# Kernel tuning notes

Measured on AMD Instinct MI355X. Metric: run time of the kernel, lower is better.

Reference implementation:

```python
import jax, jax.numpy as jnp
import numpy as np

HEADS = 4
DIM_HEAD = 32
EPS = 1e-5

def _layernorm(x, g, b):
    mu = jnp.mean(x, axis=-1, keepdims=True)
    var = jnp.var(x, axis=-1, keepdims=True)
    return (x - mu) * jax.lax.rsqrt(var + EPS) * g + b

def setup_inputs() -> dict:
    key = jax.random.key(0)
    ks = jax.random.split(key, 8)
    B, C, H, W = 16, 256, 32, 32
    N = H * W
    inner = HEADS * DIM_HEAD  # 128
    s = lambda d: 1.0 / np.sqrt(d)
    return {
        "x": jax.random.normal(ks[0], (B, C, H, W), jnp.float32),
        "pos_embedding": jax.random.normal(ks[1], (1, N, C), jnp.float32),
        "w_qkv": jax.random.normal(ks[2], (C, inner * 3), jnp.float32) * s(C),
        "w_out": jax.random.normal(ks[3], (inner, C), jnp.float32) * s(inner),
        "b_out": jnp.zeros((C,), jnp.float32),
        "w_ff1": jax.random.normal(ks[4], (C, inner), jnp.float32) * s(C),
        "b_ff1": jnp.zeros((inner,), jnp.float32),
        "w_ff2": jax.random.normal(ks[5], (inner, C), jnp.float32) * s(inner),
        "b_ff2": jnp.zeros((C,), jnp.float32),
        "g1": jnp.ones((C,), jnp.float32),
        "beta1": jnp.zeros((C,), jnp.float32),
        "g2": jnp.ones((C,), jnp.float32),
        "beta2": jnp.zeros((C,), jnp.float32),
    }

def reference(x, pos_embedding, w_qkv, w_out, b_out, w_ff1, b_ff1, w_ff2, b_ff2, g1, beta1, g2, beta2):
    b, c, h, w = x.shape
    n = h * w
    tok = jnp.transpose(x.reshape(b, c, n), (0, 2, 1))  # [b, n, c]
    tok = tok + pos_embedding  # (dropout is identity at eval)
    # attention
    qkv = _layernorm(tok, g1, beta1) @ w_qkv  # [b, n, 3*inner]
    qkv = qkv.reshape(b, n, 3, HEADS, DIM_HEAD)
    q, k, v = qkv[:, :, 0], qkv[:, :, 1], qkv[:, :, 2]  # [b, n, h, d]
    scale = DIM_HEAD ** -0.5
    dots = jnp.einsum('bihd,bjhd->bhij', q, k) * scale
    attn = jax.nn.softmax(dots, axis=-1)
    out = jnp.einsum('bhij,bjhd->bihd', attn, v).reshape(b, n, HEADS * DIM_HEAD)
    tok = out @ w_out + b_out + tok
    # ffn
    hdn = jax.nn.gelu(_layernorm(tok, g2, beta2) @ w_ff1 + b_ff1, approximate=False)
    tok = hdn @ w_ff2 + b_ff2 + tok
    return jnp.transpose(tok, (0, 2, 1)).reshape(b, c, h, w)
```

## Files before the change

### kernel.cpp

```cpp
#include <hip/hip_runtime.h>
#include <hip/hip_bf16.h>
#include <math.h>

#define B_     16
#define C_     256
#define N_     1024
#define HEADS_ 4
#define DH_    32
#define INNER_ 128
#define EPS_   1e-5f

typedef __attribute__((ext_vector_type(8))) short bf16x8;
typedef __attribute__((ext_vector_type(4))) float f32x4;

__device__ __forceinline__ ushort f2bf(float f) {
  union { float f; unsigned u; } v; v.f = f;
  unsigned u = v.u;
  return (ushort)((u + 0x7fffu + ((u >> 16) & 1u)) >> 16);
}
__device__ __forceinline__ float bf2f(ushort u) {
  union { unsigned u; float f; } v; v.u = ((unsigned)u) << 16;
  return v.f;
}
__device__ __forceinline__ unsigned cvt_pk_bf16(float lo, float hi) {
  unsigned r;
  asm("v_cvt_pk_bf16_f32 %0, %1, %2" : "=v"(r) : "v"(lo), "v"(hi));
  return r;
}

#define QSCALE_ 0.2550348652979437f

__global__ __launch_bounds__(256) void k_wconv(
    const float* __restrict__ wqkv, const float* __restrict__ wout,
    const float* __restrict__ wff1, const float* __restrict__ wff2,
    ushort* __restrict__ wqkvT, ushort* __restrict__ woutT,
    ushort* __restrict__ wff1T, ushort* __restrict__ wff2T) {
  int i = blockIdx.x * 256 + threadIdx.x;
  if (i < 98304) {
    int k = i / 384, n = i % 384;
    wqkvT[n * 256 + k] = f2bf(wqkv[i]);
    return;
  }
  i -= 98304;
  if (i < 32768) {
    int k = i / 256, n = i % 256;
    woutT[n * 128 + k] = f2bf(wout[i]);
    return;
  }
  i -= 32768;
  if (i < 32768) {
    int k = i / 128, n = i % 128;
    wff1T[n * 256 + k] = f2bf(wff1[i]);
    return;
  }
  i -= 32768;
  {
    int k = i / 256, n = i % 256;
    wff2T[n * 128 + k] = f2bf(wff2[i]);
  }
}

union KFusedSmem {
  float  xs[C_][68];
  ushort xnl[64][264];
};

__global__ __launch_bounds__(512) void k_fused(
    const float* __restrict__ x, const float* __restrict__ pos,
    const float* __restrict__ g1, const float* __restrict__ beta1,
    const ushort* __restrict__ wqkvT, ushort* __restrict__ tokb,
    ushort* __restrict__ qb, ushort* __restrict__ kb, ushort* __restrict__ vtb) {
  const int b  = blockIdx.x >> 4;
  const int n0 = (blockIdx.x & 15) << 6;
  const int t  = threadIdx.x;
  __shared__ KFusedSmem u;

  {
    const int nq = t & 15, cq = t >> 4;
#pragma unroll
    for (int i = 0; i < 8; ++i) {
      const int c = i * 32 + cq;
      const float4 v = *reinterpret_cast<const float4*>(
          &x[((size_t)b * C_ + c) * N_ + n0 + 4 * nq]);
      *reinterpret_cast<float4*>(&u.xs[c][4 * nq]) = v;
    }
  }
  __syncthreads();

  {
    const int tl = t >> 3, sub = t & 7, c0 = sub * 32;
    const int n = n0 + tl;
    float v[32];
#pragma unroll
    for (int i = 0; i < 32; ++i) v[i] = u.xs[c0 + i][tl];
#pragma unroll
    for (int j = 0; j < 8; ++j) {
      const float4 p = *reinterpret_cast<const float4*>(&pos[(size_t)n * C_ + c0 + 4 * j]);
      v[4*j] += p.x; v[4*j+1] += p.y; v[4*j+2] += p.z; v[4*j+3] += p.w;
    }
    float s = 0.f;
#pragma unroll
    for (int i = 0; i < 32; ++i) s += v[i];
    s += __shfl_xor(s, 1); s += __shfl_xor(s, 2); s += __shfl_xor(s, 4);
    const float mu = s * (1.f / C_);
    float sq = 0.f;
#pragma unroll
    for (int i = 0; i < 32; ++i) { const float d = v[i] - mu; sq += d * d; }
    sq += __shfl_xor(sq, 1); sq += __shfl_xor(sq, 2); sq += __shfl_xor(sq, 4);
    const float rs = rsqrtf(sq * (1.f / C_) + EPS_);

    ushort* tokrow = &tokb[((size_t)b * N_ + n) * C_ + c0];
    ushort xn_local[32];
#pragma unroll
    for (int j = 0; j < 8; ++j) {
      ushort4 tu;
      tu.x = f2bf(v[4*j]);   tu.y = f2bf(v[4*j+1]);
      tu.z = f2bf(v[4*j+2]); tu.w = f2bf(v[4*j+3]);
      *reinterpret_cast<ushort4*>(&tokrow[4 * j]) = tu;
      const float4 g  = *reinterpret_cast<const float4*>(&g1[c0 + 4 * j]);
      const float4 be = *reinterpret_cast<const float4*>(&beta1[c0 + 4 * j]);
      xn_local[4*j]   = f2bf((v[4*j]   - mu) * rs * g.x + be.x);
      xn_local[4*j+1] = f2bf((v[4*j+1] - mu) * rs * g.y + be.y);
      xn_local[4*j+2] = f2bf((v[4*j+2] - mu) * rs * g.z + be.z);
      xn_local[4*j+3] = f2bf((v[4*j+3] - mu) * rs * g.w + be.w);
    }
    __syncthreads();
#pragma unroll
    for (int j = 0; j < 8; ++j)
      *reinterpret_cast<ushort4*>(&u.xnl[tl][c0 + 4 * j]) =
          *reinterpret_cast<ushort4*>(&xn_local[4 * j]);
  }
  __syncthreads();

  {
    const int w = t >> 6, lane = t & 63;
    const int li = lane & 15, g = lane >> 4;
#pragma unroll
    for (int mf = 0; mf < 3; ++mf) {
      const int chb = w * 48 + mf * 16;
      bf16x8 Af[8];
#pragma unroll
      for (int ks = 0; ks < 8; ++ks)
        Af[ks] = *reinterpret_cast<const bf16x8*>(
            &wqkvT[(size_t)(chb + li) * C_ + ks * 32 + 8 * g]);
#pragma unroll
      for (int nf = 0; nf < 4; ++nf) {
        bf16x8 Bf[8];
#pragma unroll
        for (int ks = 0; ks < 8; ++ks)
          Bf[ks] = *reinterpret_cast<const bf16x8*>(&u.xnl[nf * 16 + li][ks * 32 + 8 * g]);
        f32x4 acc = {0.f, 0.f, 0.f, 0.f};
#pragma unroll
        for (int ks = 0; ks < 8; ++ks)
          acc = __builtin_amdgcn_mfma_f32_16x16x32_bf16(Af[ks], Bf[ks], acc, 0, 0, 0);
        const int nn = n0 + nf * 16 + li;
        const int ch0 = chb + 4 * g;
        if (ch0 < 128) {
          const int h = ch0 >> 5, dh = ch0 & 31;
          ushort4 uq;
          uq.x = f2bf(acc[0] * QSCALE_); uq.y = f2bf(acc[1] * QSCALE_);
          uq.z = f2bf(acc[2] * QSCALE_); uq.w = f2bf(acc[3] * QSCALE_);
          *reinterpret_cast<ushort4*>(&qb[(((size_t)(b * HEADS_ + h)) * N_ + nn) * DH_ + dh]) = uq;
        } else if (ch0 < 256) {
          const int c2 = ch0 - 128, h = c2 >> 5, dh = c2 & 31;
          ushort4 uk;
          uk.x = f2bf(acc[0]); uk.y = f2bf(acc[1]); uk.z = f2bf(acc[2]); uk.w = f2bf(acc[3]);
          *reinterpret_cast<ushort4*>(&kb[(((size_t)(b * HEADS_ + h)) * N_ + nn) * DH_ + dh]) = uk;
        } else {
          const int c2 = ch0 - 256, h = c2 >> 5, dh = c2 & 31;
          ushort* base = &vtb[(((size_t)(b * HEADS_ + h)) * DH_ + dh) * N_ + nn];
          base[0] = f2bf(acc[0]); base[N_] = f2bf(acc[1]);
          base[2 * N_] = f2bf(acc[2]); base[3 * N_] = f2bf(acc[3]);
        }
      }
    }
  }
}

__global__ __launch_bounds__(256) void k_attn_mlp(
    const ushort* __restrict__ qb, const ushort* __restrict__ kb,
    const ushort* __restrict__ vtb, const ushort* __restrict__ tokb,
    const ushort* __restrict__ woutT, const float* __restrict__ b_out,
    const ushort* __restrict__ wff1T, const float* __restrict__ b_ff1,
    const ushort* __restrict__ wff2T, const float* __restrict__ b_ff2,
    const float* __restrict__ g2, const float* __restrict__ beta2,
    float* __restrict__ out) {
  const int b   = blockIdx.x >> 5;
  const int tt  = blockIdx.x & 31;
  const int nq0 = tt * 32;
  const int tid = threadIdx.x;
  const int w = tid >> 6, lane = tid & 63;
  const int qi = lane & 15, g = lane >> 4;

  __shared__ __align__(16) union {
    ushort P[4][2][16][72];
    float  t2s[32][260];
  } u1;
  __shared__ __align__(16) ushort xn2[32][264];
  __shared__ __align__(16) union {
    ushort aos[32][136];
    ushort hsb[32][136];
  } u2;

  {
    const int bh = b * HEADS_ + w;
    const ushort* Kb = kb  + (size_t)bh * N_ * DH_;
    const ushort* Vt = vtb + (size_t)bh * DH_ * N_;

    bf16x8 qf[2];
#pragma unroll
    for (int G = 0; G < 2; ++G)
      qf[G] = *reinterpret_cast<const bf16x8*>(
          qb + ((size_t)bh * N_ + nq0 + G * 16 + qi) * DH_ + 8 * g);

    f32x4 acc[2][2];
#pragma unroll
    for (int G = 0; G < 2; ++G)
#pragma unroll
      for (int d = 0; d < 2; ++d)
#pragma unroll
        for (int r = 0; r < 4; ++r) acc[G][d][r] = 0.f;
    float l[2] = {0.f, 0.f};

    bf16x8 kf[4], vf[2][2];
#pragma unroll
    for (int kt = 0; kt < 4; ++kt)
      kf[kt] = *reinterpret_cast<const bf16x8*>(
          Kb + (size_t)(kt * 16 + qi) * DH_ + 8 * g);
#pragma unroll
    for (int c = 0; c < 2; ++c)
#pragma unroll
      for (int d = 0; d < 2; ++d)
        vf[c][d] = *reinterpret_cast<const bf16x8*>(
            Vt + (size_t)(d * 16 + qi) * N_ + c * 32 + 8 * g);

    for (int jt = 0; jt < 16; ++jt) {
      const int kn = (jt < 15 ? jt + 1 : 15) * 64;
      bf16x8 kfn[4], vfn[2][2];
#pragma unroll
      for (int kt = 0; kt < 4; ++kt)
        kfn[kt] = *reinterpret_cast<const bf16x8*>(
            Kb + (size_t)(kn + kt * 16 + qi) * DH_ + 8 * g);
#pragma unroll
      for (int c = 0; c < 2; ++c)
#pragma unroll
        for (int d = 0; d < 2; ++d)
          vfn[c][d] = *reinterpret_cast<const bf16x8*>(
              Vt + (size_t)(d * 16 + qi) * N_ + kn + c * 32 + 8 * g);

      f32x4 s[2][4];
#pragma unroll
      for (int G = 0; G < 2; ++G)
#pragma unroll
        for (int kt = 0; kt < 4; ++kt) {
          f32x4 z = {0.f, 0.f, 0.f, 0.f};
          s[G][kt] = __builtin_amdgcn_mfma_f32_16x16x32_bf16(kf[kt], qf[G], z, 0, 0, 0);
        }

#pragma unroll
      for (int G = 0; G < 2; ++G) {
        float psum = 0.f;
#pragma unroll
        for (int kt = 0; kt < 4; ++kt) {
          const float p0 = exp2f(s[G][kt][0]);
          const float p1 = exp2f(s[G][kt][1]);
          const float p2 = exp2f(s[G][kt][2]);
          const float p3 = exp2f(s[G][kt][3]);
          psum += (p0 + p1) + (p2 + p3);
          uint2 dw;
          dw.x = cvt_pk_bf16(p0, p1);
          dw.y = cvt_pk_bf16(p2, p3);
          *reinterpret_cast<uint2*>(&u1.P[w][G][qi][kt * 16 + 4 * g]) = dw;
        }
        l[G] += psum;
      }

#pragma unroll
      for (int c = 0; c < 2; ++c) {
        const bf16x8 pf0 = *reinterpret_cast<const bf16x8*>(&u1.P[w][0][qi][c * 32 + 8 * g]);
        const bf16x8 pf1 = *reinterpret_cast<const bf16x8*>(&u1.P[w][1][qi][c * 32 + 8 * g]);
#pragma unroll
        for (int d = 0; d < 2; ++d) {
          acc[0][d] = __builtin_amdgcn_mfma_f32_16x16x32_bf16(vf[c][d], pf0, acc[0][d], 0, 0, 0);
          acc[1][d] = __builtin_amdgcn_mfma_f32_16x16x32_bf16(vf[c][d], pf1, acc[1][d], 0, 0, 0);
        }
      }

#pragma unroll
      for (int kt = 0; kt < 4; ++kt) kf[kt] = kfn[kt];
#pragma unroll
      for (int c = 0; c < 2; ++c)
#pragma unroll
        for (int d = 0; d < 2; ++d) vf[c][d] = vfn[c][d];
    }

#pragma unroll
    for (int G = 0; G < 2; ++G) {
      float lg = l[G];
      lg += __shfl_xor(lg, 16);
      lg += __shfl_xor(lg, 32);
      const float inv = 1.f / lg;
      const int nloc = G * 16 + qi;
#pragma unroll
      for (int d = 0; d < 2; ++d) {
        ushort4 uo;
        uo.x = f2bf(acc[G][d][0] * inv);
        uo.y = f2bf(acc[G][d][1] * inv);
        uo.z = f2bf(acc[G][d][2] * inv);
        uo.w = f2bf(acc[G][d][3] * inv);
        *reinterpret_cast<ushort4*>(&u2.aos[nloc][w * 32 + d * 16 + 4 * g]) = uo;
      }
    }
  }
  __syncthreads();

  const int li = qi;

  {
    bf16x8 Af[2][4];
#pragma unroll
    for (int mf = 0; mf < 2; ++mf)
#pragma unroll
      for (int ks = 0; ks < 4; ++ks)
        Af[mf][ks] = *reinterpret_cast<const bf16x8*>(&u2.aos[mf * 16 + li][ks * 32 + 8 * g]);
#pragma unroll
    for (int nf = 0; nf < 4; ++nf) {
      const int n = w * 64 + nf * 16;
      bf16x8 Bf[4];
#pragma unroll
      for (int ks = 0; ks < 4; ++ks)
        Bf[ks] = *reinterpret_cast<const bf16x8*>(
            &woutT[(size_t)(n + li) * INNER_ + ks * 32 + 8 * g]);
#pragma unroll
      for (int mf = 0; mf < 2; ++mf) {
        f32x4 acc = {0.f, 0.f, 0.f, 0.f};
#pragma unroll
        for (int ks = 0; ks < 4; ++ks)
          acc = __builtin_amdgcn_mfma_f32_16x16x32_bf16(Af[mf][ks], Bf[ks], acc, 0, 0, 0);
        const int nch = n + li;
        const int tl0 = mf * 16 + 4 * g;
        const float bo = b_out[nch];
#pragma unroll
        for (int r = 0; r < 4; ++r)
          u1.t2s[tl0 + r][nch] =
              acc[r] + bo + bf2f(tokb[((size_t)b * N_ + nq0 + tl0 + r) * C_ + nch]);
      }
    }
  }
  __syncthreads();

  {
    const int tl = tid >> 3, c0 = (tid & 7) * 32;
    float v[32];
#pragma unroll
    for (int j = 0; j < 8; ++j) {
      const float4 t4 = *reinterpret_cast<const float4*>(&u1.t2s[tl][c0 + 4 * j]);
      v[4*j] = t4.x; v[4*j+1] = t4.y; v[4*j+2] = t4.z; v[4*j+3] = t4.w;
    }
    float s = 0.f;
#pragma unroll
    for (int i = 0; i < 32; ++i) s += v[i];
    s += __shfl_xor(s, 1); s += __shfl_xor(s, 2); s += __shfl_xor(s, 4);
    const float mu = s * (1.f / C_);
    float sq = 0.f;
#pragma unroll
    for (int i = 0; i < 32; ++i) { const float d = v[i] - mu; sq += d * d; }
    sq += __shfl_xor(sq, 1); sq += __shfl_xor(sq, 2); sq += __shfl_xor(sq, 4);
    const float rs = rsqrtf(sq * (1.f / C_) + EPS_);
#pragma unroll
    for (int j = 0; j < 8; ++j) {
      const float4 gg = *reinterpret_cast<const float4*>(&g2[c0 + 4 * j]);
      const float4 be = *reinterpret_cast<const float4*>(&beta2[c0 + 4 * j]);
      ushort4 uu;
      uu.x = f2bf((v[4*j]   - mu) * rs * gg.x + be.x);
      uu.y = f2bf((v[4*j+1] - mu) * rs * gg.y + be.y);
      uu.z = f2bf((v[4*j+2] - mu) * rs * gg.z + be.z);
      uu.w = f2bf((v[4*j+3] - mu) * rs * gg.w + be.w);
      *reinterpret_cast<ushort4*>(&xn2[tl][c0 + 4 * j]) = uu;
    }
  }
  __syncthreads();

  {
    bf16x8 Af[2][8];
#pragma unroll
    for (int mf = 0; mf < 2; ++mf)
#pragma unroll
      for (int ks = 0; ks < 8; ++ks)
        Af[mf][ks] = *reinterpret_cast<const bf16x8*>(&xn2[mf * 16 + li][ks * 32 + 8 * g]);
#pragma unroll
    for (int nf = 0; nf < 2; ++nf) {
      const int n = w * 32 + nf * 16;
      bf16x8 Bf[8];
#pragma unroll
      for (int ks = 0; ks < 8; ++ks)
        Bf[ks] = *reinterpret_cast<const bf16x8*>(
            &wff1T[(size_t)(n + li) * C_ + ks * 32 + 8 * g]);
#pragma unroll
      for (int mf = 0; mf < 2; ++mf) {
        f32x4 acc = {0.f, 0.f, 0.f, 0.f};
#pragma unroll
        for (int ks = 0; ks < 8; ++ks)
          acc = __builtin_amdgcn_mfma_f32_16x16x32_bf16(Af[mf][ks], Bf[ks], acc, 0, 0, 0);
        const int nch = n + li;
        const int tl0 = mf * 16 + 4 * g;
        const float bf1 = b_ff1[nch];
#pragma unroll
        for (int r = 0; r < 4; ++r) {
          float hv = acc[r] + bf1;
          hv = 0.5f * hv * (1.f + erff(hv * 0.70710678118654752f));
          u2.hsb[tl0 + r][nch] = f2bf(hv);
        }
      }
    }
  }
  __syncthreads();

  {
    bf16x8 Af[2][4];
#pragma unroll
    for (int mf = 0; mf < 2; ++mf)
#pragma unroll
      for (int ks = 0; ks < 4; ++ks)
        Af[mf][ks] = *reinterpret_cast<const bf16x8*>(&u2.hsb[mf * 16 + li][ks * 32 + 8 * g]);
#pragma unroll
    for (int nf = 0; nf < 4; ++nf) {
      const int n = w * 64 + nf * 16;
      bf16x8 Bf[4];
#pragma unroll
      for (int ks = 0; ks < 4; ++ks)
        Bf[ks] = *reinterpret_cast<const bf16x8*>(
            &wff2T[(size_t)(n + li) * INNER_ + ks * 32 + 8 * g]);
#pragma unroll
      for (int mf = 0; mf < 2; ++mf) {
        f32x4 acc = {0.f, 0.f, 0.f, 0.f};
#pragma unroll
        for (int ks = 0; ks < 4; ++ks)
          acc = __builtin_amdgcn_mfma_f32_16x16x32_bf16(Af[mf][ks], Bf[ks], acc, 0, 0, 0);
        const int nch = n + li;
        const int tl0 = mf * 16 + 4 * g;
        const float bo = b_ff2[nch];
        float4 o;
        o.x = acc[0] + bo + u1.t2s[tl0 + 0][nch];
        o.y = acc[1] + bo + u1.t2s[tl0 + 1][nch];
        o.z = acc[2] + bo + u1.t2s[tl0 + 2][nch];
        o.w = acc[3] + bo + u1.t2s[tl0 + 3][nch];
        *reinterpret_cast<float4*>(
            &out[((size_t)b * C_ + nch) * N_ + nq0 + tl0]) = o;
      }
    }
  }
}

extern "C" void kernel_launch(void* const* d_in, const int* in_sizes, int n_in,
                              void* d_out, int out_size, void* d_ws, size_t ws_size,
                              hipStream_t stream) {
  const float* x     = (const float*)d_in[0];
  const float* pos   = (const float*)d_in[1];
  const float* w_qkv = (const float*)d_in[2];
  const float* w_out = (const float*)d_in[3];
  const float* b_out = (const float*)d_in[4];
  const float* w_ff1 = (const float*)d_in[5];
  const float* b_ff1 = (const float*)d_in[6];
  const float* w_ff2 = (const float*)d_in[7];
  const float* b_ff2 = (const float*)d_in[8];
  const float* g1    = (const float*)d_in[9];
  const float* beta1 = (const float*)d_in[10];
  const float* g2    = (const float*)d_in[11];
  const float* beta2 = (const float*)d_in[12];
  float* out = (float*)d_out;

  ushort* tokb  = (ushort*)d_ws;
  ushort* qb    = tokb + 4194304;
  ushort* kb    = qb + 2097152;
  ushort* vtb   = kb + 2097152;
  ushort* wqkvT = vtb + 2097152;
  ushort* woutT = wqkvT + 98304;
  ushort* wff1T = woutT + 32768;
  ushort* wff2T = wff1T + 32768;

  k_wconv<<<768, 256, 0, stream>>>(w_qkv, w_out, w_ff1, w_ff2,
                                   wqkvT, woutT, wff1T, wff2T);
  k_fused<<<256, 512, 0, stream>>>(x, pos, g1, beta1, wqkvT, tokb, qb, kb, vtb);
  k_attn_mlp<<<512, 256, 0, stream>>>(qb, kb, vtb, tokb, woutT, b_out,
                                      wff1T, b_ff1, wff2T, b_ff2, g2, beta2, out);
}
```

Measured before the change: 153.8 us.

## Halve query tile per block to 16 rows and drop K/V register prefetch

```diff
diff --git a/kernel.cpp b/kernel.cpp
--- a/kernel.cpp
+++ b/kernel.cpp
@@ -185,21 +185,21 @@
     const ushort* __restrict__ wff2T, const float* __restrict__ b_ff2,
     const float* __restrict__ g2, const float* __restrict__ beta2,
     float* __restrict__ out) {
-  const int b   = blockIdx.x >> 5;
-  const int tt  = blockIdx.x & 31;
-  const int nq0 = tt * 32;
+  const int b   = blockIdx.x >> 6;
+  const int tt  = blockIdx.x & 63;
+  const int nq0 = tt * 16;
   const int tid = threadIdx.x;
   const int w = tid >> 6, lane = tid & 63;
   const int qi = lane & 15, g = lane >> 4;
 
   __shared__ __align__(16) union {
-    ushort P[4][2][16][72];
-    float  t2s[32][260];
+    ushort P[4][16][72];
+    float  t2s[16][260];
   } u1;
-  __shared__ __align__(16) ushort xn2[32][264];
+  __shared__ __align__(16) ushort xn2[16][264];
   __shared__ __align__(16) union {
-    ushort aos[32][136];
-    ushort hsb[32][136];
+    ushort aos[16][136];
+    ushort hsb[16][136];
   } u2;
 
   {
@@ -207,109 +207,67 @@
     const ushort* Kb = kb  + (size_t)bh * N_ * DH_;
     const ushort* Vt = vtb + (size_t)bh * DH_ * N_;
 
-    bf16x8 qf[2];
-#pragma unroll
-    for (int G = 0; G < 2; ++G)
-      qf[G] = *reinterpret_cast<const bf16x8*>(
-          qb + ((size_t)bh * N_ + nq0 + G * 16 + qi) * DH_ + 8 * g);
-
-    f32x4 acc[2][2];
-#pragma unroll
-    for (int G = 0; G < 2; ++G)
-#pragma unroll
-      for (int d = 0; d < 2; ++d)
-#pragma unroll
-        for (int r = 0; r < 4; ++r) acc[G][d][r] = 0.f;
-    float l[2] = {0.f, 0.f};
-
-    bf16x8 kf[4], vf[2][2];
-#pragma unroll
-    for (int kt = 0; kt < 4; ++kt)
-      kf[kt] = *reinterpret_cast<const bf16x8*>(
-          Kb + (size_t)(kt * 16 + qi) * DH_ + 8 * g);
-#pragma unroll
-    for (int c = 0; c < 2; ++c)
-#pragma unroll
-      for (int d = 0; d < 2; ++d)
-        vf[c][d] = *reinterpret_cast<const bf16x8*>(
-            Vt + (size_t)(d * 16 + qi) * N_ + c * 32 + 8 * g);
+    const bf16x8 qf = *reinterpret_cast<const bf16x8*>(
+        qb + ((size_t)bh * N_ + nq0 + qi) * DH_ + 8 * g);
+
+    f32x4 acc[2];
+#pragma unroll
+    for (int d = 0; d < 2; ++d)
+#pragma unroll
+      for (int r = 0; r < 4; ++r) acc[d][r] = 0.f;
+    float l = 0.f;
 
     for (int jt = 0; jt < 16; ++jt) {
-      const int kn = (jt < 15 ? jt + 1 : 15) * 64;
-      bf16x8 kfn[4], vfn[2][2];
-#pragma unroll
-      for (int kt = 0; kt < 4; ++kt)
-        kfn[kt] = *reinterpret_cast<const bf16x8*>(
-            Kb + (size_t)(kn + kt * 16 + qi) * DH_ + 8 * g);
-#pragma unroll
-      for (int c = 0; c < 2; ++c)
-#pragma unroll
-        for (int d = 0; d < 2; ++d)
-          vfn[c][d] = *reinterpret_cast<const bf16x8*>(
-              Vt + (size_t)(d * 16 + qi) * N_ + kn + c * 32 + 8 * g);
-
-      f32x4 s[2][4];
-#pragma unroll
-      for (int G = 0; G < 2; ++G)
-#pragma unroll
-        for (int kt = 0; kt < 4; ++kt) {
-          f32x4 z = {0.f, 0.f, 0.f, 0.f};
-          s[G][kt] = __builtin_amdgcn_mfma_f32_16x16x32_bf16(kf[kt], qf[G], z, 0, 0, 0);
-        }
-
-#pragma unroll
-      for (int G = 0; G < 2; ++G) {
-        float psum = 0.f;
-#pragma unroll
-        for (int kt = 0; kt < 4; ++kt) {
-          const float p0 = exp2f(s[G][kt][0]);
-          const float p1 = exp2f(s[G][kt][1]);
-          const float p2 = exp2f(s[G][kt][2]);
-          const float p3 = exp2f(s[G][kt][3]);
-          psum += (p0 + p1) + (p2 + p3);
-          uint2 dw;
-          dw.x = cvt_pk_bf16(p0, p1);
-          dw.y = cvt_pk_bf16(p2, p3);
-          *reinterpret_cast<uint2*>(&u1.P[w][G][qi][kt * 16 + 4 * g]) = dw;
-        }
-        l[G] += psum;
+      const int k0 = jt * 64;
+
+      f32x4 s[4];
+#pragma unroll
+      for (int kt = 0; kt < 4; ++kt) {
+        const bf16x8 kf = *reinterpret_cast<const bf16x8*>(
+            Kb + (size_t)(k0 + kt * 16 + qi) * DH_ + 8 * g);
+        f32x4 z = {0.f, 0.f, 0.f, 0.f};
+        s[kt] = __builtin_amdgcn_mfma_f32_16x16x32_bf16(kf, qf, z, 0, 0, 0);
       }
 
+      float psum = 0.f;
+#pragma unroll
+      for (int kt = 0; kt < 4; ++kt) {
+        const float p0 = exp2f(s[kt][0]);
+        const float p1 = exp2f(s[kt][1]);
+        const float p2 = exp2f(s[kt][2]);
+        const float p3 = exp2f(s[kt][3]);
+        psum += (p0 + p1) + (p2 + p3);
+        uint2 dw;
+        dw.x = cvt_pk_bf16(p0, p1);
+        dw.y = cvt_pk_bf16(p2, p3);
+        *reinterpret_cast<uint2*>(&u1.P[w][qi][kt * 16 + 4 * g]) = dw;
+      }
+      l += psum;
+
 #pragma unroll
       for (int c = 0; c < 2; ++c) {
-        const bf16x8 pf0 = *reinterpret_cast<const bf16x8*>(&u1.P[w][0][qi][c * 32 + 8 * g]);
-        const bf16x8 pf1 = *reinterpret_cast<const bf16x8*>(&u1.P[w][1][qi][c * 32 + 8 * g]);
+        const bf16x8 pf = *reinterpret_cast<const bf16x8*>(&u1.P[w][qi][c * 32 + 8 * g]);
 #pragma unroll
         for (int d = 0; d < 2; ++d) {
-          acc[0][d] = __builtin_amdgcn_mfma_f32_16x16x32_bf16(vf[c][d], pf0, acc[0][d], 0, 0, 0);
-          acc[1][d] = __builtin_amdgcn_mfma_f32_16x16x32_bf16(vf[c][d], pf1, acc[1][d], 0, 0, 0);
+          const bf16x8 vf = *reinterpret_cast<const bf16x8*>(
+              Vt + (size_t)(d * 16 + qi) * N_ + k0 + c * 32 + 8 * g);
+          acc[d] = __builtin_amdgcn_mfma_f32_16x16x32_bf16(vf, pf, acc[d], 0, 0, 0);
         }
       }
-
-#pragma unroll
-      for (int kt = 0; kt < 4; ++kt) kf[kt] = kfn[kt];
-#pragma unroll
-      for (int c = 0; c < 2; ++c)
-#pragma unroll
-        for (int d = 0; d < 2; ++d) vf[c][d] = vfn[c][d];
-    }
-
-#pragma unroll
-    for (int G = 0; G < 2; ++G) {
-      float lg = l[G];
-      lg += __shfl_xor(lg, 16);
-      lg += __shfl_xor(lg, 32);
-      const float inv = 1.f / lg;
-      const int nloc = G * 16 + qi;
-#pragma unroll
-      for (int d = 0; d < 2; ++d) {
-        ushort4 uo;
-        uo.x = f2bf(acc[G][d][0] * inv);
-        uo.y = f2bf(acc[G][d][1] * inv);
-        uo.z = f2bf(acc[G][d][2] * inv);
-        uo.w = f2bf(acc[G][d][3] * inv);
-        *reinterpret_cast<ushort4*>(&u2.aos[nloc][w * 32 + d * 16 + 4 * g]) = uo;
-      }
+    }
+
+    float lg = l;
+    lg += __shfl_xor(lg, 16);
+    lg += __shfl_xor(lg, 32);
+    const float inv = 1.f / lg;
+#pragma unroll
+    for (int d = 0; d < 2; ++d) {
+      ushort4 uo;
+      uo.x = f2bf(acc[d][0] * inv);
+      uo.y = f2bf(acc[d][1] * inv);
+      uo.z = f2bf(acc[d][2] * inv);
+      uo.w = f2bf(acc[d][3] * inv);
+      *reinterpret_cast<ushort4*>(&u2.aos[qi][w * 32 + d * 16 + 4 * g]) = uo;
     }
   }
   __syncthreads();
@@ -317,12 +275,10 @@
   const int li = qi;
 
   {
-    bf16x8 Af[2][4];
-#pragma unroll
-    for (int mf = 0; mf < 2; ++mf)
-#pragma unroll
-      for (int ks = 0; ks < 4; ++ks)
-        Af[mf][ks] = *reinterpret_cast<const bf16x8*>(&u2.aos[mf * 16 + li][ks * 32 + 8 * g]);
+    bf16x8 Af[4];
+#pragma unroll
+    for (int ks = 0; ks < 4; ++ks)
+      Af[ks] = *reinterpret_cast<const bf16x8*>(&u2.aos[li][ks * 32 + 8 * g]);
 #pragma unroll
     for (int nf = 0; nf < 4; ++nf) {
       const int n = w * 64 + nf * 16;
@@ -331,44 +287,43 @@
       for (int ks = 0; ks < 4; ++ks)
         Bf[ks] = *reinterpret_cast<const bf16x8*>(
             &woutT[(size_t)(n + li) * INNER_ + ks * 32 + 8 * g]);
-#pragma unroll
-      for (int mf = 0; mf < 2; ++mf) {
-        f32x4 acc = {0.f, 0.f, 0.f, 0.f};
-#pragma unroll
-        for (int ks = 0; ks < 4; ++ks)
-          acc = __builtin_amdgcn_mfma_f32_16x16x32_bf16(Af[mf][ks], Bf[ks], acc, 0, 0, 0);
-        const int nch = n + li;
-        const int tl0 = mf * 16 + 4 * g;
-        const float bo = b_out[nch];
-#pragma unroll
-        for (int r = 0; r < 4; ++r)
-          u1.t2s[tl0 + r][nch] =
-              acc[r] + bo + bf2f(tokb[((size_t)b * N_ + nq0 + tl0 + r) * C_ + nch]);
-      }
-    }
-  }
-  __syncthreads();
-
-  {
-    const int tl = tid >> 3, c0 = (tid & 7) * 32;
-    float v[32];
-#pragma unroll
-    for (int j = 0; j < 8; ++j) {
+      f32x4 acc = {0.f, 0.f, 0.f, 0.f};
+#pragma unroll
+      for (int ks = 0; ks < 4; ++ks)
+        acc = __builtin_amdgcn_mfma_f32_16x16x32_bf16(Af[ks], Bf[ks], acc, 0, 0, 0);
+      const int nch = n + li;
+      const int tl0 = 4 * g;
+      const float bo = b_out[nch];
+#pragma unroll
+      for (int r = 0; r < 4; ++r)
+        u1.t2s[tl0 + r][nch] =
+            acc[r] + bo + bf2f(tokb[((size_t)b * N_ + nq0 + tl0 + r) * C_ + nch]);
+    }
+  }
+  __syncthreads();
+
+  {
+    const int tl = tid >> 4, c0 = (tid & 15) * 16;
+    float v[16];
+#pragma unroll
+    for (int j = 0; j < 4; ++j) {
       const float4 t4 = *reinterpret_cast<const float4*>(&u1.t2s[tl][c0 + 4 * j]);
       v[4*j] = t4.x; v[4*j+1] = t4.y; v[4*j+2] = t4.z; v[4*j+3] = t4.w;
     }
     float s = 0.f;
 #pragma unroll
-    for (int i = 0; i < 32; ++i) s += v[i];
-    s += __shfl_xor(s, 1); s += __shfl_xor(s, 2); s += __shfl_xor(s, 4);
+    for (int i = 0; i < 16; ++i) s += v[i];
+    s += __shfl_xor(s, 1); s += __shfl_xor(s, 2);
+    s += __shfl_xor(s, 4); s += __shfl_xor(s, 8);
     const float mu = s * (1.f / C_);
     float sq = 0.f;
 #pragma unroll
-    for (int i = 0; i < 32; ++i) { const float d = v[i] - mu; sq += d * d; }
-    sq += __shfl_xor(sq, 1); sq += __shfl_xor(sq, 2); sq += __shfl_xor(sq, 4);
+    for (int i = 0; i < 16; ++i) { const float d = v[i] - mu; sq += d * d; }
+    sq += __shfl_xor(sq, 1); sq += __shfl_xor(sq, 2);
+    sq += __shfl_xor(sq, 4); sq += __shfl_xor(sq, 8);
     const float rs = rsqrtf(sq * (1.f / C_) + EPS_);
 #pragma unroll
-    for (int j = 0; j < 8; ++j) {
+    for (int j = 0; j < 4; ++j) {
       const float4 gg = *reinterpret_cast<const float4*>(&g2[c0 + 4 * j]);
       const float4 be = *reinterpret_cast<const float4*>(&beta2[c0 + 4 * j]);
       ushort4 uu;
@@ -382,12 +337,10 @@
   __syncthreads();
 
   {
-    bf16x8 Af[2][8];
-#pragma unroll
-    for (int mf = 0; mf < 2; ++mf)
-#pragma unroll
-      for (int ks = 0; ks < 8; ++ks)
-        Af[mf][ks] = *reinterpret_cast<const bf16x8*>(&xn2[mf * 16 + li][ks * 32 + 8 * g]);
+    bf16x8 Af[8];
+#pragma unroll
+    for (int ks = 0; ks < 8; ++ks)
+      Af[ks] = *reinterpret_cast<const bf16x8*>(&xn2[li][ks * 32 + 8 * g]);
 #pragma unroll
     for (int nf = 0; nf < 2; ++nf) {
       const int n = w * 32 + nf * 16;
@@ -396,33 +349,28 @@
       for (int ks = 0; ks < 8; ++ks)
         Bf[ks] = *reinterpret_cast<const bf16x8*>(
             &wff1T[(size_t)(n + li) * C_ + ks * 32 + 8 * g]);
-#pragma unroll
-      for (int mf = 0; mf < 2; ++mf) {
-        f32x4 acc = {0.f, 0.f, 0.f, 0.f};
-#pragma unroll
-        for (int ks = 0; ks < 8; ++ks)
-          acc = __builtin_amdgcn_mfma_f32_16x16x32_bf16(Af[mf][ks], Bf[ks], acc, 0, 0, 0);
-        const int nch = n + li;
-        const int tl0 = mf * 16 + 4 * g;
-        const float bf1 = b_ff1[nch];
-#pragma unroll
-        for (int r = 0; r < 4; ++r) {
-          float hv = acc[r] + bf1;
-          hv = 0.5f * hv * (1.f + erff(hv * 0.70710678118654752f));
-          u2.hsb[tl0 + r][nch] = f2bf(hv);
-        }
+      f32x4 acc = {0.f, 0.f, 0.f, 0.f};
+#pragma unroll
+      for (int ks = 0; ks < 8; ++ks)
+        acc = __builtin_amdgcn_mfma_f32_16x16x32_bf16(Af[ks], Bf[ks], acc, 0, 0, 0);
+      const int nch = n + li;
+      const int tl0 = 4 * g;
+      const float bf1 = b_ff1[nch];
+#pragma unroll
+      for (int r = 0; r < 4; ++r) {
+        float hv = acc[r] + bf1;
+        hv = 0.5f * hv * (1.f + erff(hv * 0.70710678118654752f));
+        u2.hsb[tl0 + r][nch] = f2bf(hv);
       }
     }
   }
   __syncthreads();
 
   {
-    bf16x8 Af[2][4];
-#pragma unroll
-    for (int mf = 0; mf < 2; ++mf)
-#pragma unroll
-      for (int ks = 0; ks < 4; ++ks)
-        Af[mf][ks] = *reinterpret_cast<const bf16x8*>(&u2.hsb[mf * 16 + li][ks * 32 + 8 * g]);
+    bf16x8 Af[4];
+#pragma unroll
+    for (int ks = 0; ks < 4; ++ks)
+      Af[ks] = *reinterpret_cast<const bf16x8*>(&u2.hsb[li][ks * 32 + 8 * g]);
 #pragma unroll
     for (int nf = 0; nf < 4; ++nf) {
       const int n = w * 64 + nf * 16;
@@ -431,23 +379,20 @@
       for (int ks = 0; ks < 4; ++ks)
         Bf[ks] = *reinterpret_cast<const bf16x8*>(
             &wff2T[(size_t)(n + li) * INNER_ + ks * 32 + 8 * g]);
-#pragma unroll
-      for (int mf = 0; mf < 2; ++mf) {
-        f32x4 acc = {0.f, 0.f, 0.f, 0.f};
-#pragma unroll
-        for (int ks = 0; ks < 4; ++ks)
-          acc = __builtin_amdgcn_mfma_f32_16x16x32_bf16(Af[mf][ks], Bf[ks], acc, 0, 0, 0);
-        const int nch = n + li;
-        const int tl0 = mf * 16 + 4 * g;
-        const float bo = b_ff2[nch];
-        float4 o;
-        o.x = acc[0] + bo + u1.t2s[tl0 + 0][nch];
-        o.y = acc[1] + bo + u1.t2s[tl0 + 1][nch];
-        o.z = acc[2] + bo + u1.t2s[tl0 + 2][nch];
-        o.w = acc[3] + bo + u1.t2s[tl0 + 3][nch];
-        *reinterpret_cast<float4*>(
-            &out[((size_t)b * C_ + nch) * N_ + nq0 + tl0]) = o;
-      }
+      f32x4 acc = {0.f, 0.f, 0.f, 0.f};
+#pragma unroll
+      for (int ks = 0; ks < 4; ++ks)
+        acc = __builtin_amdgcn_mfma_f32_16x16x32_bf16(Af[ks], Bf[ks], acc, 0, 0, 0);
+      const int nch = n + li;
+      const int tl0 = 4 * g;
+      const float bo = b_ff2[nch];
+      float4 o;
+      o.x = acc[0] + bo + u1.t2s[tl0 + 0][nch];
+      o.y = acc[1] + bo + u1.t2s[tl0 + 1][nch];
+      o.z = acc[2] + bo + u1.t2s[tl0 + 2][nch];
+      o.w = acc[3] + bo + u1.t2s[tl0 + 3][nch];
+      *reinterpret_cast<float4*>(
+          &out[((size_t)b * C_ + nch) * N_ + nq0 + tl0]) = o;
     }
   }
 }
@@ -482,6 +427,6 @@
   k_wconv<<<768, 256, 0, stream>>>(w_qkv, w_out, w_ff1, w_ff2,
                                    wqkvT, woutT, wff1T, wff2T);
   k_fused<<<256, 512, 0, stream>>>(x, pos, g1, beta1, wqkvT, tokb, qb, kb, vtb);
-  k_attn_mlp<<<512, 256, 0, stream>>>(qb, kb, vtb, tokb, woutT, b_out,
-                                      wff1T, b_ff1, wff2T, b_ff2, g2, beta2, out);
-}
+  k_attn_mlp<<<1024, 256, 0, stream>>>(qb, kb, vtb, tokb, woutT, b_out,
+                                       wff1T, b_ff1, wff2T, b_ff2, g2, beta2, out);
+}
```

Measured after the change: 181.7 us. 1.18x slower.
